# Kernel optimization log

Measured on AMD Instinct MI355X. Metric: run time of the kernel, lower is better.

The kernel has to match this reference:

```python
import jax, jax.numpy as jnp
import numpy as np

N = 20000      # num nodes
E = 320000     # num edges (avg degree 16)
F_IN = 518     # object_feature_dim
D = 128        # node_embedding_dim (= GAT out_channels)
ED = 32        # edge_embedding_dim
R = 26         # num_relations
H = 4          # GAT heads (concat=False -> mean over heads)
HID = 256      # node_encoder hidden


def _gat_layer(x, src, dst, ea, lin, lin_e, att_s, att_d, att_e, bias):
    """PyG GATConv: add_self_loops=True (fill_value='mean'), concat=False, negative_slope=0.2."""
    n = x.shape[0]
    ones = jnp.ones((src.shape[0],), x.dtype)
    cnt = jax.ops.segment_sum(ones, dst, num_segments=n)                    # [N]
    loop_ea = jax.ops.segment_sum(ea, dst, num_segments=n) / jnp.maximum(cnt, 1.0)[:, None]
    idx = jnp.arange(n)
    s = jnp.concatenate([src, idx])
    d = jnp.concatenate([dst, idx])
    ea2 = jnp.concatenate([ea, loop_ea], axis=0)                            # [E+N, ED]
    h = (x @ lin).reshape(n, H, D)                                          # [N,H,D]
    a_s = jnp.einsum('nhd,hd->nh', h, att_s)                                # [N,H]
    a_d = jnp.einsum('nhd,hd->nh', h, att_d)
    e = (ea2 @ lin_e).reshape(-1, H, D)                                     # [E+N,H,D]
    a_e = jnp.einsum('ehd,hd->eh', e, att_e)
    alpha = jax.nn.leaky_relu(a_s[s] + a_d[d] + a_e, 0.2)                   # [E+N,H]
    amax = jax.ops.segment_max(alpha, d, num_segments=n)
    alpha = jnp.exp(alpha - amax[d])
    denom = jax.ops.segment_sum(alpha, d, num_segments=n)
    alpha = alpha / (denom[d] + 1e-16)                                      # segment softmax
    msg = h[s] * alpha[:, :, None]                                          # [E+N,H,D]
    out = jax.ops.segment_sum(msg, d, num_segments=n)                       # [N,H,D]
    return out.mean(axis=1) + bias                                          # concat=False


def setup_inputs() -> dict:
    key = jax.random.key(0)
    ks = jax.random.split(key, 18)
    g = lambda k, shp, s=0.05: jax.random.normal(k, shp, jnp.float32) * s
    return {
        'x': g(ks[0], (N, F_IN), 1.0),
        'edge_index': jax.random.randint(ks[1], (2, E), 0, N),
        'edge_type': jax.random.randint(ks[2], (E,), 0, R),
        'w1': g(ks[3], (F_IN, HID)), 'b1': jnp.zeros((HID,), jnp.float32),
        'w2': g(ks[4], (HID, D)),    'b2': jnp.zeros((D,), jnp.float32),
        'rel_emb': g(ks[5], (R, ED), 1.0),
        'lin1': g(ks[6], (D, H * D)), 'line1': g(ks[7], (ED, H * D)),
        'atts1': g(ks[8], (H, D)), 'attd1': g(ks[9], (H, D)), 'atte1': g(ks[10], (H, D)),
        'bias1': jnp.zeros((D,), jnp.float32),
        'lin2': g(ks[11], (D, H * D)), 'line2': g(ks[12], (ED, H * D)),
        'atts2': g(ks[13], (H, D)), 'attd2': g(ks[14], (H, D)), 'atte2': g(ks[15], (H, D)),
        'bias2': jnp.zeros((D,), jnp.float32),
    }


def reference(x, edge_index, edge_type, w1, b1, w2, b2, rel_emb,
              lin1, line1, atts1, attd1, atte1, bias1,
              lin2, line2, atts2, attd2, atte2, bias2):
    src, dst = edge_index[0], edge_index[1]
    # node encoder (dropout inactive in eval)
    h = jax.nn.relu(x @ w1 + b1) @ w2 + b2                                  # [N,D]
    ea = rel_emb[edge_type]                                                 # [E,ED]
    h = jax.nn.relu(_gat_layer(h, src, dst, ea, lin1, line1, atts1, attd1, atte1, bias1))
    h = jax.nn.relu(_gat_layer(h, src, dst, ea, lin2, line2, atts2, attd2, atte2, bias2))
    return h
```

## Files before the change

### kernel.cpp

```cpp
#include <hip/hip_runtime.h>
#include <math.h>

#define N_NODES 20000
#define MP      20032
#define N_EDGES 320000
#define F_IN    518
#define HIDDEN  256
#define DIM     128
#define NH      4

typedef __attribute__((ext_vector_type(8))) short bf16x8;
typedef __attribute__((ext_vector_type(4))) float f32x4;
typedef unsigned short ushort_t;

__device__ __forceinline__ float lrelu02(float x) { return x > 0.f ? x : 0.2f * x; }

__device__ __forceinline__ void gl_lds16(const void* g, void* l) {
    __builtin_amdgcn_global_load_lds(
        (const __attribute__((address_space(1))) unsigned int*)g,
        (__attribute__((address_space(3))) unsigned int*)l, 16, 0, 0);
}

__device__ __forceinline__ unsigned int hi16(float v) { return __float_as_uint(v) >> 16; }
__device__ __forceinline__ unsigned int lo16(float v) {
    unsigned int h = __float_as_uint(v) & 0xFFFF0000u;
    return __float_as_uint(v - __uint_as_float(h)) >> 16;
}
__device__ __forceinline__ unsigned int rnd16(float v) {
    unsigned int u = __float_as_uint(v);
    return (u + 0x7FFFu + ((u >> 16) & 1u)) >> 16;
}
__device__ __forceinline__ float bfl(unsigned int u) { return __uint_as_float(u << 16); }
__device__ __forceinline__ float bfh(unsigned int u) { return __uint_as_float(u & 0xFFFF0000u); }

__global__ __launch_bounds__(256, 4) void gemm_mfma_v2(
    const ushort_t* __restrict__ Ah, const ushort_t* __restrict__ Al,
    const ushort_t* __restrict__ Bh, const ushort_t* __restrict__ Bl,
    const float* __restrict__ bias,
    int M, int K8, int N, int act,
    float* __restrict__ Cf,
    ushort_t* __restrict__ Ch, ushort_t* __restrict__ Cl,
    ushort_t* __restrict__ Cb,
    ushort_t* __restrict__ Ca)
{
    __shared__ __align__(16) ushort_t lds[12288];
    const int tid = threadIdx.x;
    const int w = tid >> 6, lane = tid & 63;
    const int row0 = blockIdx.y * 64, col0 = blockIdx.x * 128;
    const int nkb = K8 >> 2;
    const int m16 = lane & 15, q = lane >> 4;
    const bool use_al = (Al != nullptr);

    f32x4 acc[4][2] = {};

    for (int kb = 0; kb < nkb; ++kb) {
        const size_t kc = (size_t)(kb * 4 + w);
        const size_t aoff = (kc * MP + row0) * 8 + lane * 8;
        const size_t boff = (kc * N + col0) * 8 + lane * 8;
        gl_lds16(Ah + aoff, &lds[w * 512]);
        if (use_al) gl_lds16(Al + aoff, &lds[2048 + w * 512]);
        gl_lds16(Bh + boff,       &lds[4096 + w * 1024]);
        gl_lds16(Bh + boff + 512, &lds[4096 + w * 1024 + 512]);
        gl_lds16(Bl + boff,       &lds[8192 + w * 1024]);
        gl_lds16(Bl + boff + 512, &lds[8192 + w * 1024 + 512]);
        __syncthreads();

        bf16x8 fah[4], fal[4], fbh[2], fbl[2];
        const int fa = q * 512 + m16 * 8;
        #pragma unroll
        for (int mi = 0; mi < 4; ++mi) {
            fah[mi] = *(const bf16x8*)&lds[fa + mi * 128];
            if (use_al) fal[mi] = *(const bf16x8*)&lds[2048 + fa + mi * 128];
        }
        const int fb = q * 1024 + (w * 32 + m16) * 8;
        #pragma unroll
        for (int ni = 0; ni < 2; ++ni) {
            fbh[ni] = *(const bf16x8*)&lds[4096 + fb + ni * 128];
            fbl[ni] = *(const bf16x8*)&lds[8192 + fb + ni * 128];
        }
        #pragma unroll
        for (int mi = 0; mi < 4; ++mi)
            #pragma unroll
            for (int ni = 0; ni < 2; ++ni) {
                acc[mi][ni] = __builtin_amdgcn_mfma_f32_16x16x32_bf16(fah[mi], fbh[ni], acc[mi][ni], 0, 0, 0);
                acc[mi][ni] = __builtin_amdgcn_mfma_f32_16x16x32_bf16(fah[mi], fbl[ni], acc[mi][ni], 0, 0, 0);
            }
        if (use_al) {
            #pragma unroll
            for (int mi = 0; mi < 4; ++mi)
                #pragma unroll
                for (int ni = 0; ni < 2; ++ni)
                    acc[mi][ni] = __builtin_amdgcn_mfma_f32_16x16x32_bf16(fal[mi], fbh[ni], acc[mi][ni], 0, 0, 0);
        }
        __syncthreads();
    }

    #pragma unroll
    for (int ni = 0; ni < 2; ++ni) {
        const int col = col0 + w * 32 + ni * 16 + m16;
        const float bb = bias ? bias[col] : 0.f;
        #pragma unroll
        for (int mi = 0; mi < 4; ++mi) {
            #pragma unroll
            for (int r = 0; r < 4; ++r) {
                const int row = row0 + mi * 16 + q * 4 + r;
                if (row < M) {
                    float v = acc[mi][ni][r] + bb;
                    if (act) v = fmaxf(v, 0.f);
                    if (Cf) Cf[(size_t)row * N + col] = v;
                    if (Cb) Cb[(size_t)row * N + col] = (ushort_t)rnd16(v);
                    const size_t p = (((size_t)(col >> 3)) * MP + row) * 8 + (col & 7);
                    if (Ch) { Ch[p] = (ushort_t)hi16(v); Cl[p] = (ushort_t)lo16(v); }
                    if (Ca) Ca[p] = (ushort_t)rnd16(v);
                }
            }
        }
    }
}

__global__ __launch_bounds__(256) void conv_a_t_kernel(
    const float* __restrict__ x, ushort_t* __restrict__ xh, ushort_t* __restrict__ xl)
{
    __shared__ float tile[64][68];
    const int tid = threadIdx.x;
    const int r0 = blockIdx.x * 64;
    const int c0 = blockIdx.y * 64;

    #pragma unroll
    for (int it = 0; it < 4; ++it) {
        const int r = (tid >> 4) + it * 16;
        const int c = (tid & 15) * 4;
        const int gr = r0 + r, gc = c0 + c;
        float4 v = {0.f, 0.f, 0.f, 0.f};
        if (gr < N_NODES) {
            if (gc + 3 < F_IN) {
                v = *(const float4*)(x + (size_t)gr * F_IN + gc);
            } else {
                float tmp[4] = {0.f, 0.f, 0.f, 0.f};
                #pragma unroll
                for (int u = 0; u < 4; ++u)
                    if (gc + u < F_IN) tmp[u] = x[(size_t)gr * F_IN + gc + u];
                v.x = tmp[0]; v.y = tmp[1]; v.z = tmp[2]; v.w = tmp[3];
            }
        }
        tile[r][c] = v.x; tile[r][c+1] = v.y; tile[r][c+2] = v.z; tile[r][c+3] = v.w;
    }
    __syncthreads();

    const int k8l = tid >> 5;
    const int k8 = (c0 >> 3) + k8l;
    if (k8 >= 68) return;
    const int rr = (tid & 31) * 2;
    #pragma unroll
    for (int u = 0; u < 2; ++u) {
        const int r = rr + u;
        unsigned int hp[4], lp[4];
        #pragma unroll
        for (int i = 0; i < 4; ++i) {
            const float v0 = tile[r][k8l * 8 + 2 * i];
            const float v1 = tile[r][k8l * 8 + 2 * i + 1];
            hp[i] = (hi16(v1) << 16) | hi16(v0);
            lp[i] = (lo16(v1) << 16) | lo16(v0);
        }
        const size_t p = ((size_t)k8 * MP + r0 + r) * 8;
        *(uint4*)(xh + p) = make_uint4(hp[0], hp[1], hp[2], hp[3]);
        *(uint4*)(xl + p) = make_uint4(lp[0], lp[1], lp[2], lp[3]);
    }
}

__global__ __launch_bounds__(256) void conv_b_kernel(
    const float* __restrict__ w, ushort_t* __restrict__ bh, ushort_t* __restrict__ bl,
    int K, int N, int total)
{
    const int idx = blockIdx.x * 256 + threadIdx.x;
    if (idx >= total) return;
    const int j = idx & 7;
    const int rem = idx >> 3;
    const int n = rem % N;
    const int k = (rem / N) * 8 + j;
    const float v = (k < K) ? w[(size_t)k * N + n] : 0.f;
    bh[idx] = (ushort_t)hi16(v);
    bl[idx] = (ushort_t)lo16(v);
}

__global__ __launch_bounds__(256) void wa_kernel(
    const float* __restrict__ lin, const float* __restrict__ atts,
    const float* __restrict__ attd, float* __restrict__ wa_s, float* __restrict__ wa_d)
{
    const int wrk = blockIdx.x * 256 + threadIdx.x;
    if (wrk >= 1024) return;
    const int sd = wrk >> 9;
    const int p = wrk & 511;
    const int h = p >> 7, d = p & 127;
    const float* av = (sd ? attd : atts) + h * DIM;
    const float* lp = lin + (size_t)d * (NH * DIM) + h * DIM;
    float acc = 0.f;
    #pragma unroll 8
    for (int i = 0; i < DIM; ++i) acc += lp[i] * av[i];
    (sd ? wa_d : wa_s)[h * DIM + d] = acc;
}

__global__ __launch_bounds__(256) void as_ad_kernel(
    const float* __restrict__ xb, const float* __restrict__ wa_s,
    const float* __restrict__ wa_d, float* __restrict__ a_s, float* __restrict__ a_d)
{
    const int gw = blockIdx.x * 4 + (threadIdx.x >> 6);
    const int lane = threadIdx.x & 63;
    if (gw >= N_NODES * NH) return;
    const int n = gw >> 2, h = gw & 3;
    const float* hp = xb + (size_t)n * DIM;
    float2 hv = *(const float2*)(hp + lane * 2);
    float2 sv = *(const float2*)(wa_s + h * DIM + lane * 2);
    float2 dv = *(const float2*)(wa_d + h * DIM + lane * 2);
    float s = hv.x * sv.x + hv.y * sv.y;
    float d = hv.x * dv.x + hv.y * dv.y;
    #pragma unroll
    for (int off = 32; off > 0; off >>= 1) {
        s += __shfl_down(s, off);
        d += __shfl_down(d, off);
    }
    if (lane == 0) { a_s[n * 4 + h] = s; a_d[n * 4 + h] = d; }
}

__global__ __launch_bounds__(128) void rel_table_kernel(
    const float* __restrict__ rel_emb, const float* __restrict__ line,
    const float* __restrict__ atte, float* __restrict__ table)
{
    __shared__ float we[32][NH];
    const int tid = threadIdx.x;
    const int k = tid >> 2, h = tid & 3;
    float acc = 0.f;
    for (int d = 0; d < DIM; ++d)
        acc += line[(size_t)k * (NH * DIM) + h * DIM + d] * atte[h * DIM + d];
    we[k][h] = acc;
    __syncthreads();
    if (tid < 26 * NH) {
        int r = tid >> 2, hh = tid & 3;
        float t = 0.f;
        for (int kk = 0; kk < 32; ++kk) t += rel_emb[r * 32 + kk] * we[kk][hh];
        table[r * 4 + hh] = t;
    }
}

__global__ __launch_bounds__(256) void hist_kernel(
    const int* __restrict__ dst, int* __restrict__ cnt)
{
    const int e = blockIdx.x * blockDim.x + threadIdx.x;
    if (e >= N_EDGES) return;
    atomicAdd(&cnt[dst[e]], 1);
}

__global__ __launch_bounds__(1024) void scan_kernel(
    const int* __restrict__ cnt, int* __restrict__ ptr, int* __restrict__ ptr_copy)
{
    __shared__ int tsum[1024];
    const int tid = threadIdx.x;
    const int CH = 20;
    const int base = tid * CH;
    int s = 0;
    #pragma unroll
    for (int i = 0; i < CH; ++i) {
        int idx = base + i;
        if (idx < N_NODES) s += cnt[idx];
    }
    tsum[tid] = s;
    __syncthreads();
    for (int off = 1; off < 1024; off <<= 1) {
        int v = (tid >= off) ? tsum[tid - off] : 0;
        __syncthreads();
        tsum[tid] += v;
        __syncthreads();
    }
    int run = (tid == 0) ? 0 : tsum[tid - 1];
    #pragma unroll
    for (int i = 0; i < CH; ++i) {
        int idx = base + i;
        if (idx < N_NODES) {
            ptr[idx] = run;
            ptr_copy[idx] = run;
            run += cnt[idx];
        }
    }
    if (tid == 0) ptr[N_NODES] = N_EDGES;
}

__global__ __launch_bounds__(256) void scatter_kernel(
    const int* __restrict__ src, const int* __restrict__ dst, const int* __restrict__ etype,
    int* __restrict__ ptr_copy, int2* __restrict__ se)
{
    const int e = blockIdx.x * blockDim.x + threadIdx.x;
    if (e >= N_EDGES) return;
    const int d = dst[e];
    const int pos = atomicAdd(&ptr_copy[d], 1);
    se[pos] = make_int2(src[e], etype[e]);
}

__global__ __launch_bounds__(256) void node_agg_kernel(
    const int* __restrict__ ptr, const int2* __restrict__ se,
    const float* __restrict__ a_s, const float* __restrict__ a_d,
    const float* __restrict__ table, const ushort_t* __restrict__ hb,
    const float* __restrict__ bias,
    float* __restrict__ outf, ushort_t* __restrict__ oa,
    const float* __restrict__ wa_s2, const float* __restrict__ wa_d2,
    float* __restrict__ a_s2, float* __restrict__ a_d2)
{
    const int n = blockIdx.x * 4 + (threadIdx.x >> 6);
    const int lane = threadIdx.x & 63;
    if (n >= N_NODES) return;
    const int beg = ptr[n], end = ptr[n + 1];
    const int head = lane >> 4;
    const int cbase = lane * 8;
    const float adh = a_d[n * 4 + head];

    float acc[8] = {};
    float dh = 0.f, eh = 0.f;

    int j = beg;
    for (; j + 4 <= end; j += 4) {
        int2 E[4];
        E[0] = se[j]; E[1] = se[j + 1]; E[2] = se[j + 2]; E[3] = se[j + 3];
        uint4 g[4];
        float av[4], tv[4];
        #pragma unroll
        for (int u = 0; u < 4; ++u) {
            g[u] = *(const uint4*)(hb + (size_t)E[u].x * 512 + cbase);
            av[u] = a_s[E[u].x * 4 + head];
            tv[u] = table[E[u].y * 4 + head];
        }
        #pragma unroll
        for (int u = 0; u < 4; ++u) {
            const float p = __expf(lrelu02(av[u] + adh + tv[u]));
            eh += tv[u]; dh += p;
            acc[0] += p * bfl(g[u].x); acc[1] += p * bfh(g[u].x);
            acc[2] += p * bfl(g[u].y); acc[3] += p * bfh(g[u].y);
            acc[4] += p * bfl(g[u].z); acc[5] += p * bfh(g[u].z);
            acc[6] += p * bfl(g[u].w); acc[7] += p * bfh(g[u].w);
        }
    }
    for (; j < end; ++j) {
        const int2 E0 = se[j];
        const uint4 g0 = *(const uint4*)(hb + (size_t)E0.x * 512 + cbase);
        const float a0 = a_s[E0.x * 4 + head];
        const float t0 = table[E0.y * 4 + head];
        const float p0 = __expf(lrelu02(a0 + adh + t0));
        eh += t0; dh += p0;
        acc[0] += p0 * bfl(g0.x); acc[1] += p0 * bfh(g0.x);
        acc[2] += p0 * bfl(g0.y); acc[3] += p0 * bfh(g0.y);
        acc[4] += p0 * bfl(g0.z); acc[5] += p0 * bfh(g0.z);
        acc[6] += p0 * bfl(g0.w); acc[7] += p0 * bfh(g0.w);
    }

    const float inv = 1.0f / fmaxf((float)(end - beg), 1.0f);
    const float ps = __expf(lrelu02(a_s[n * 4 + head] + adh + eh * inv));
    dh += ps;
    {
        const uint4 gs = *(const uint4*)(hb + (size_t)n * 512 + cbase);
        acc[0] += ps * bfl(gs.x); acc[1] += ps * bfh(gs.x);
        acc[2] += ps * bfl(gs.y); acc[3] += ps * bfh(gs.y);
        acc[4] += ps * bfl(gs.z); acc[5] += ps * bfh(gs.z);
        acc[6] += ps * bfl(gs.w); acc[7] += ps * bfh(gs.w);
    }

    const float ih = 0.25f / (dh + 1e-16f);
    float t[8];
    #pragma unroll
    for (int k = 0; k < 8; ++k) {
        t[k] = acc[k] * ih;
        t[k] += __shfl_xor(t[k], 16);
        t[k] += __shfl_xor(t[k], 32);
    }
    if (lane < 16) {
        const float4 b0 = *(const float4*)(bias + cbase);
        const float4 b1 = *(const float4*)(bias + cbase + 4);
        float o[8];
        o[0] = fmaxf(t[0] + b0.x, 0.f); o[1] = fmaxf(t[1] + b0.y, 0.f);
        o[2] = fmaxf(t[2] + b0.z, 0.f); o[3] = fmaxf(t[3] + b0.w, 0.f);
        o[4] = fmaxf(t[4] + b1.x, 0.f); o[5] = fmaxf(t[5] + b1.y, 0.f);
        o[6] = fmaxf(t[6] + b1.z, 0.f); o[7] = fmaxf(t[7] + b1.w, 0.f);
        if (outf) {
            float4 v0 = {o[0], o[1], o[2], o[3]};
            float4 v1 = {o[4], o[5], o[6], o[7]};
            *(float4*)(outf + (size_t)n * DIM + cbase) = v0;
            *(float4*)(outf + (size_t)n * DIM + cbase + 4) = v1;
        }
        if (oa) {
            unsigned int up[4];
            #pragma unroll
            for (int i = 0; i < 4; ++i)
                up[i] = (rnd16(o[2*i+1]) << 16) | rnd16(o[2*i]);
            *(uint4*)(oa + ((size_t)lane * MP + n) * 8) = make_uint4(up[0], up[1], up[2], up[3]);
        }
        if (wa_s2) {
            float pss[4] = {0,0,0,0}, pdd[4] = {0,0,0,0};
            #pragma unroll
            for (int h = 0; h < NH; ++h) {
                const float* ws = wa_s2 + h * DIM + cbase;
                const float* wd = wa_d2 + h * DIM + cbase;
                #pragma unroll
                for (int i = 0; i < 8; ++i) {
                    pss[h] += o[i] * ws[i];
                    pdd[h] += o[i] * wd[i];
                }
            }
            #pragma unroll
            for (int m = 1; m < 16; m <<= 1) {
                #pragma unroll
                for (int h = 0; h < NH; ++h) {
                    pss[h] += __shfl_xor(pss[h], m);
                    pdd[h] += __shfl_xor(pdd[h], m);
                }
            }
            if (lane == 0) {
                float4 vs = {pss[0], pss[1], pss[2], pss[3]};
                float4 vd = {pdd[0], pdd[1], pdd[2], pdd[3]};
                *(float4*)(a_s2 + n * 4) = vs;
                *(float4*)(a_d2 + n * 4) = vd;
            }
        }
    }
}

extern "C" void kernel_launch(void* const* d_in, const int* in_sizes, int n_in,
                              void* d_out, int out_size, void* d_ws, size_t ws_size,
                              hipStream_t stream)
{
    const float* x       = (const float*)d_in[0];
    const int*   eidx    = (const int*)d_in[1];
    const int*   etype   = (const int*)d_in[2];
    const float* w1      = (const float*)d_in[3];
    const float* b1      = (const float*)d_in[4];
    const float* w2      = (const float*)d_in[5];
    const float* b2      = (const float*)d_in[6];
    const float* rel_emb = (const float*)d_in[7];
    const float* lin[2]  = {(const float*)d_in[8],  (const float*)d_in[14]};
    const float* line[2] = {(const float*)d_in[9],  (const float*)d_in[15]};
    const float* atts[2] = {(const float*)d_in[10], (const float*)d_in[16]};
    const float* attd[2] = {(const float*)d_in[11], (const float*)d_in[17]};
    const float* atte[2] = {(const float*)d_in[12], (const float*)d_in[18]};
    const float* bias[2] = {(const float*)d_in[13], (const float*)d_in[19]};
    const int* src = eidx;
    const int* dst = eidx + N_EDGES;

    char* base = (char*)d_ws;
    size_t off = 0;
    auto alloc = [&](size_t bytes) -> void* {
        void* p = base + off;
        off = (off + bytes + 255) & ~(size_t)255;
        return p;
    };
    ushort_t* xh  = (ushort_t*)alloc((size_t)68 * MP * 8 * 2);
    ushort_t* xl  = (ushort_t*)alloc((size_t)68 * MP * 8 * 2);
    ushort_t* h1h = (ushort_t*)alloc((size_t)32 * MP * 8 * 2);
    ushort_t* h1l = (ushort_t*)alloc((size_t)32 * MP * 8 * 2);
    ushort_t* x0a = (ushort_t*)alloc((size_t)16 * MP * 8 * 2);
    void* reg1    = alloc((size_t)16 * MP * 8 * 4);
    ushort_t* w1h = (ushort_t*)alloc(68 * 256 * 8 * 2);
    ushort_t* w1l = (ushort_t*)alloc(68 * 256 * 8 * 2);
    ushort_t* w2h = (ushort_t*)alloc(32 * 128 * 8 * 2);
    ushort_t* w2l = (ushort_t*)alloc(32 * 128 * 8 * 2);
    ushort_t* l0h = (ushort_t*)alloc(16 * 512 * 8 * 2);
    ushort_t* l0l = (ushort_t*)alloc(16 * 512 * 8 * 2);
    ushort_t* l1h = (ushort_t*)alloc(16 * 512 * 8 * 2);
    ushort_t* l1l = (ushort_t*)alloc(16 * 512 * 8 * 2);
    float* a_s0  = (float*)alloc(N_NODES * 4 * 4);
    float* a_d0  = (float*)alloc(N_NODES * 4 * 4);
    float* a_s1  = (float*)alloc(N_NODES * 4 * 4);
    float* a_d1  = (float*)alloc(N_NODES * 4 * 4);
    float* table = (float*)alloc(128 * 4);
    float* wa_s0 = (float*)alloc(512 * 4);
    float* wa_d0 = (float*)alloc(512 * 4);
    float* wa_s1 = (float*)alloc(512 * 4);
    float* wa_d1 = (float*)alloc(512 * 4);
    int*  cnt_i  = (int*)alloc(N_NODES * 4);
    int*  ptr    = (int*)alloc((N_NODES + 4) * 4);
    int*  ptrc   = (int*)alloc(N_NODES * 4);
    int2* se     = (int2*)alloc((size_t)N_EDGES * 8);

    ushort_t* hb = xh;
    float* xbuf0 = (float*)reg1;
    ushort_t* x1a = (ushort_t*)reg1;

    const int mtiles = MP / 64;

    conv_a_t_kernel<<<dim3(MP / 64, 9), 256, 0, stream>>>(x, xh, xl);
    conv_b_kernel<<<(68*256*8 + 255) / 256, 256, 0, stream>>>(w1, w1h, w1l, F_IN, HIDDEN, 68*256*8);
    conv_b_kernel<<<(32*128*8 + 255) / 256, 256, 0, stream>>>(w2, w2h, w2l, HIDDEN, DIM, 32*128*8);
    conv_b_kernel<<<(16*512*8 + 255) / 256, 256, 0, stream>>>(lin[0], l0h, l0l, DIM, NH*DIM, 16*512*8);
    conv_b_kernel<<<(16*512*8 + 255) / 256, 256, 0, stream>>>(lin[1], l1h, l1l, DIM, NH*DIM, 16*512*8);
    wa_kernel<<<4, 256, 0, stream>>>(lin[0], atts[0], attd[0], wa_s0, wa_d0);
    wa_kernel<<<4, 256, 0, stream>>>(lin[1], atts[1], attd[1], wa_s1, wa_d1);

    hipMemsetAsync(cnt_i, 0, N_NODES * sizeof(int), stream);
    hist_kernel<<<(N_EDGES + 255) / 256, 256, 0, stream>>>(dst, cnt_i);
    scan_kernel<<<1, 1024, 0, stream>>>(cnt_i, ptr, ptrc);
    scatter_kernel<<<(N_EDGES + 255) / 256, 256, 0, stream>>>(src, dst, etype, ptrc, se);

    gemm_mfma_v2<<<dim3(HIDDEN / 128, mtiles), 256, 0, stream>>>(
        xh, xl, w1h, w1l, b1, N_NODES, 68, HIDDEN, 1, nullptr, h1h, h1l, nullptr, nullptr);
    gemm_mfma_v2<<<dim3(DIM / 128, mtiles), 256, 0, stream>>>(
        h1h, h1l, w2h, w2l, b2, N_NODES, 32, DIM, 0, xbuf0, nullptr, nullptr, nullptr, x0a);

    gemm_mfma_v2<<<dim3((NH * DIM) / 128, mtiles), 256, 0, stream>>>(
        x0a, nullptr, l0h, l0l, nullptr, N_NODES, 16, NH * DIM, 0, nullptr, nullptr, nullptr, hb, nullptr);
    as_ad_kernel<<<N_NODES, 256, 0, stream>>>(xbuf0, wa_s0, wa_d0, a_s0, a_d0);
    rel_table_kernel<<<1, 128, 0, stream>>>(rel_emb, line[0], atte[0], table);
    node_agg_kernel<<<(N_NODES + 3) / 4, 256, 0, stream>>>(
        ptr, se, a_s0, a_d0, table, hb, bias[0], nullptr, x1a,
        wa_s1, wa_d1, a_s1, a_d1);

    gemm_mfma_v2<<<dim3((NH * DIM) / 128, mtiles), 256, 0, stream>>>(
        x1a, nullptr, l1h, l1l, nullptr, N_NODES, 16, NH * DIM, 0, nullptr, nullptr, nullptr, hb, nullptr);
    rel_table_kernel<<<1, 128, 0, stream>>>(rel_emb, line[1], atte[1], table);
    node_agg_kernel<<<(N_NODES + 3) / 4, 256, 0, stream>>>(
        ptr, se, a_s1, a_d1, table, hb, bias[1], (float*)d_out, nullptr,
        nullptr, nullptr, nullptr, nullptr);
}
```

Measured before the change: 440.2 us.

## Split each node's edge list across two waves and batch small setup kernels

The aggregation kernel now gives each destination node two waves. Each wave handles half of the node's incoming edges, and the partial sums are combined through shared memory before the epilogue. This is meant to expose more memory-level parallelism on the gather-bound aggregation. The cost is a block barrier, LDS traffic, and the second wave idling through the epilogue. Separately, the four weight-conversion launches, the two wa launches and the two rel_table launches are merged into single launches to cut launch overhead.

```diff
diff --git a/kernel.cpp b/kernel.cpp
--- a/kernel.cpp
+++ b/kernel.cpp
@@ -168,36 +168,55 @@
     }
 }
 
-__global__ __launch_bounds__(256) void conv_b_kernel(
-    const float* __restrict__ w, ushort_t* __restrict__ bh, ushort_t* __restrict__ bl,
-    int K, int N, int total)
-{
-    const int idx = blockIdx.x * 256 + threadIdx.x;
-    if (idx >= total) return;
-    const int j = idx & 7;
-    const int rem = idx >> 3;
+#define W1_T (68 * 256 * 8)
+#define W2_T (32 * 128 * 8)
+#define L_T  (16 * 512 * 8)
+__global__ __launch_bounds__(256) void conv_w_all_kernel(
+    const float* __restrict__ w1, const float* __restrict__ w2,
+    const float* __restrict__ l0, const float* __restrict__ l1,
+    ushort_t* __restrict__ w1h, ushort_t* __restrict__ w1l,
+    ushort_t* __restrict__ w2h, ushort_t* __restrict__ w2l,
+    ushort_t* __restrict__ l0h, ushort_t* __restrict__ l0l,
+    ushort_t* __restrict__ l1h, ushort_t* __restrict__ l1l)
+{
+    int idx = blockIdx.x * 256 + threadIdx.x;
+    const float* w; ushort_t *bh, *bl; int K, N, local;
+    if (idx < W1_T) { w = w1; bh = w1h; bl = w1l; K = F_IN; N = HIDDEN; local = idx; }
+    else if (idx < W1_T + W2_T) { w = w2; bh = w2h; bl = w2l; K = HIDDEN; N = DIM; local = idx - W1_T; }
+    else if (idx < W1_T + W2_T + L_T) { w = l0; bh = l0h; bl = l0l; K = DIM; N = 512; local = idx - W1_T - W2_T; }
+    else if (idx < W1_T + W2_T + 2 * L_T) { w = l1; bh = l1h; bl = l1l; K = DIM; N = 512; local = idx - W1_T - W2_T - L_T; }
+    else return;
+    const int j = local & 7;
+    const int rem = local >> 3;
     const int n = rem % N;
     const int k = (rem / N) * 8 + j;
     const float v = (k < K) ? w[(size_t)k * N + n] : 0.f;
-    bh[idx] = (ushort_t)hi16(v);
-    bl[idx] = (ushort_t)lo16(v);
-}
-
-__global__ __launch_bounds__(256) void wa_kernel(
-    const float* __restrict__ lin, const float* __restrict__ atts,
-    const float* __restrict__ attd, float* __restrict__ wa_s, float* __restrict__ wa_d)
+    bh[local] = (ushort_t)hi16(v);
+    bl[local] = (ushort_t)lo16(v);
+}
+
+__global__ __launch_bounds__(256) void wa2_kernel(
+    const float* __restrict__ lin0, const float* __restrict__ lin1,
+    const float* __restrict__ atts0, const float* __restrict__ attd0,
+    const float* __restrict__ atts1, const float* __restrict__ attd1,
+    float* __restrict__ wa_s0, float* __restrict__ wa_d0,
+    float* __restrict__ wa_s1, float* __restrict__ wa_d1)
 {
     const int wrk = blockIdx.x * 256 + threadIdx.x;
-    if (wrk >= 1024) return;
-    const int sd = wrk >> 9;
+    if (wrk >= 2048) return;
+    const int L = wrk >> 10;
+    const int sd = (wrk >> 9) & 1;
     const int p = wrk & 511;
     const int h = p >> 7, d = p & 127;
-    const float* av = (sd ? attd : atts) + h * DIM;
+    const float* lin = L ? lin1 : lin0;
+    const float* av = L ? (sd ? attd1 : atts1) : (sd ? attd0 : atts0);
+    float* out = L ? (sd ? wa_d1 : wa_s1) : (sd ? wa_d0 : wa_s0);
     const float* lp = lin + (size_t)d * (NH * DIM) + h * DIM;
+    const float* ap = av + h * DIM;
     float acc = 0.f;
     #pragma unroll 8
-    for (int i = 0; i < DIM; ++i) acc += lp[i] * av[i];
-    (sd ? wa_d : wa_s)[h * DIM + d] = acc;
+    for (int i = 0; i < DIM; ++i) acc += lp[i] * ap[i];
+    out[h * DIM + d] = acc;
 }
 
 __global__ __launch_bounds__(256) void as_ad_kernel(
@@ -222,11 +241,17 @@
     if (lane == 0) { a_s[n * 4 + h] = s; a_d[n * 4 + h] = d; }
 }
 
-__global__ __launch_bounds__(128) void rel_table_kernel(
-    const float* __restrict__ rel_emb, const float* __restrict__ line,
-    const float* __restrict__ atte, float* __restrict__ table)
+__global__ __launch_bounds__(128) void rel_table2_kernel(
+    const float* __restrict__ rel_emb,
+    const float* __restrict__ line0, const float* __restrict__ atte0,
+    const float* __restrict__ line1, const float* __restrict__ atte1,
+    float* __restrict__ table)
 {
     __shared__ float we[32][NH];
+    const int L = blockIdx.x;
+    const float* line = L ? line1 : line0;
+    const float* atte = L ? atte1 : atte0;
+    float* tab = table + L * 128;
     const int tid = threadIdx.x;
     const int k = tid >> 2, h = tid & 3;
     float acc = 0.f;
@@ -238,7 +263,7 @@
         int r = tid >> 2, hh = tid & 3;
         float t = 0.f;
         for (int kk = 0; kk < 32; ++kk) t += rel_emb[r * 32 + kk] * we[kk][hh];
-        table[r * 4 + hh] = t;
+        tab[r * 4 + hh] = t;
     }
 }
 
@@ -295,7 +320,7 @@
     se[pos] = make_int2(src[e], etype[e]);
 }
 
-__global__ __launch_bounds__(256) void node_agg_kernel(
+__global__ __launch_bounds__(256) void node_agg2_kernel(
     const int* __restrict__ ptr, const int2* __restrict__ se,
     const float* __restrict__ a_s, const float* __restrict__ a_d,
     const float* __restrict__ table, const ushort_t* __restrict__ hb,
@@ -304,40 +329,45 @@
     const float* __restrict__ wa_s2, const float* __restrict__ wa_d2,
     float* __restrict__ a_s2, float* __restrict__ a_d2)
 {
-    const int n = blockIdx.x * 4 + (threadIdx.x >> 6);
-    const int lane = threadIdx.x & 63;
-    if (n >= N_NODES) return;
-    const int beg = ptr[n], end = ptr[n + 1];
+    __shared__ float red[2][64][11];
+    const int tid = threadIdx.x;
+    const int wave = tid >> 6, lane = tid & 63;
+    const int slot = wave >> 1, half = wave & 1;
+    const int n = blockIdx.x * 2 + slot;
     const int head = lane >> 4;
     const int cbase = lane * 8;
+    const int beg = ptr[n], end = ptr[n + 1];
+    const int mid = beg + ((end - beg + 1) >> 1);
+    const int lo = half ? mid : beg;
+    const int hi = half ? end : mid;
     const float adh = a_d[n * 4 + head];
 
     float acc[8] = {};
     float dh = 0.f, eh = 0.f;
 
-    int j = beg;
-    for (; j + 4 <= end; j += 4) {
-        int2 E[4];
-        E[0] = se[j]; E[1] = se[j + 1]; E[2] = se[j + 2]; E[3] = se[j + 3];
-        uint4 g[4];
-        float av[4], tv[4];
-        #pragma unroll
-        for (int u = 0; u < 4; ++u) {
-            g[u] = *(const uint4*)(hb + (size_t)E[u].x * 512 + cbase);
-            av[u] = a_s[E[u].x * 4 + head];
-            tv[u] = table[E[u].y * 4 + head];
-        }
-        #pragma unroll
-        for (int u = 0; u < 4; ++u) {
-            const float p = __expf(lrelu02(av[u] + adh + tv[u]));
-            eh += tv[u]; dh += p;
-            acc[0] += p * bfl(g[u].x); acc[1] += p * bfh(g[u].x);
-            acc[2] += p * bfl(g[u].y); acc[3] += p * bfh(g[u].y);
-            acc[4] += p * bfl(g[u].z); acc[5] += p * bfh(g[u].z);
-            acc[6] += p * bfl(g[u].w); acc[7] += p * bfh(g[u].w);
-        }
-    }
-    for (; j < end; ++j) {
+    int j = lo;
+    for (; j + 2 <= hi; j += 2) {
+        const int2 E0 = se[j], E1 = se[j + 1];
+        const uint4 g0 = *(const uint4*)(hb + (size_t)E0.x * 512 + cbase);
+        const uint4 g1 = *(const uint4*)(hb + (size_t)E1.x * 512 + cbase);
+        const float a0 = a_s[E0.x * 4 + head];
+        const float t0 = table[E0.y * 4 + head];
+        const float a1 = a_s[E1.x * 4 + head];
+        const float t1 = table[E1.y * 4 + head];
+        const float p0 = __expf(lrelu02(a0 + adh + t0));
+        const float p1 = __expf(lrelu02(a1 + adh + t1));
+        eh += t0 + t1;
+        dh += p0 + p1;
+        acc[0] += p0 * bfl(g0.x) + p1 * bfl(g1.x);
+        acc[1] += p0 * bfh(g0.x) + p1 * bfh(g1.x);
+        acc[2] += p0 * bfl(g0.y) + p1 * bfl(g1.y);
+        acc[3] += p0 * bfh(g0.y) + p1 * bfh(g1.y);
+        acc[4] += p0 * bfl(g0.z) + p1 * bfl(g1.z);
+        acc[5] += p0 * bfh(g0.z) + p1 * bfh(g1.z);
+        acc[6] += p0 * bfl(g0.w) + p1 * bfl(g1.w);
+        acc[7] += p0 * bfh(g0.w) + p1 * bfh(g1.w);
+    }
+    if (j < hi) {
         const int2 E0 = se[j];
         const uint4 g0 = *(const uint4*)(hb + (size_t)E0.x * 512 + cbase);
         const float a0 = a_s[E0.x * 4 + head];
@@ -349,6 +379,20 @@
         acc[4] += p0 * bfl(g0.z); acc[5] += p0 * bfh(g0.z);
         acc[6] += p0 * bfl(g0.w); acc[7] += p0 * bfh(g0.w);
     }
+
+    if (half == 1) {
+        #pragma unroll
+        for (int k = 0; k < 8; ++k) red[slot][lane][k] = acc[k];
+        red[slot][lane][8] = dh;
+        red[slot][lane][9] = eh;
+    }
+    __syncthreads();
+    if (half == 1) return;
+
+    #pragma unroll
+    for (int k = 0; k < 8; ++k) acc[k] += red[slot][lane][k];
+    dh += red[slot][lane][8];
+    eh += red[slot][lane][9];
 
     const float inv = 1.0f / fmaxf((float)(end - beg), 1.0f);
     const float ps = __expf(lrelu02(a_s[n * 4 + head] + adh + eh * inv));
@@ -454,19 +498,19 @@
     ushort_t* h1l = (ushort_t*)alloc((size_t)32 * MP * 8 * 2);
     ushort_t* x0a = (ushort_t*)alloc((size_t)16 * MP * 8 * 2);
     void* reg1    = alloc((size_t)16 * MP * 8 * 4);
-    ushort_t* w1h = (ushort_t*)alloc(68 * 256 * 8 * 2);
-    ushort_t* w1l = (ushort_t*)alloc(68 * 256 * 8 * 2);
-    ushort_t* w2h = (ushort_t*)alloc(32 * 128 * 8 * 2);
-    ushort_t* w2l = (ushort_t*)alloc(32 * 128 * 8 * 2);
-    ushort_t* l0h = (ushort_t*)alloc(16 * 512 * 8 * 2);
-    ushort_t* l0l = (ushort_t*)alloc(16 * 512 * 8 * 2);
-    ushort_t* l1h = (ushort_t*)alloc(16 * 512 * 8 * 2);
-    ushort_t* l1l = (ushort_t*)alloc(16 * 512 * 8 * 2);
+    ushort_t* w1h = (ushort_t*)alloc(W1_T * 2);
+    ushort_t* w1l = (ushort_t*)alloc(W1_T * 2);
+    ushort_t* w2h = (ushort_t*)alloc(W2_T * 2);
+    ushort_t* w2l = (ushort_t*)alloc(W2_T * 2);
+    ushort_t* l0h = (ushort_t*)alloc(L_T * 2);
+    ushort_t* l0l = (ushort_t*)alloc(L_T * 2);
+    ushort_t* l1h = (ushort_t*)alloc(L_T * 2);
+    ushort_t* l1l = (ushort_t*)alloc(L_T * 2);
     float* a_s0  = (float*)alloc(N_NODES * 4 * 4);
     float* a_d0  = (float*)alloc(N_NODES * 4 * 4);
     float* a_s1  = (float*)alloc(N_NODES * 4 * 4);
     float* a_d1  = (float*)alloc(N_NODES * 4 * 4);
-    float* table = (float*)alloc(128 * 4);
+    float* table = (float*)alloc(2 * 128 * 4);
     float* wa_s0 = (float*)alloc(512 * 4);
     float* wa_d0 = (float*)alloc(512 * 4);
     float* wa_s1 = (float*)alloc(512 * 4);
@@ -483,12 +527,11 @@
     const int mtiles = MP / 64;
 
     conv_a_t_kernel<<<dim3(MP / 64, 9), 256, 0, stream>>>(x, xh, xl);
-    conv_b_kernel<<<(68*256*8 + 255) / 256, 256, 0, stream>>>(w1, w1h, w1l, F_IN, HIDDEN, 68*256*8);
-    conv_b_kernel<<<(32*128*8 + 255) / 256, 256, 0, stream>>>(w2, w2h, w2l, HIDDEN, DIM, 32*128*8);
-    conv_b_kernel<<<(16*512*8 + 255) / 256, 256, 0, stream>>>(lin[0], l0h, l0l, DIM, NH*DIM, 16*512*8);
-    conv_b_kernel<<<(16*512*8 + 255) / 256, 256, 0, stream>>>(lin[1], l1h, l1l, DIM, NH*DIM, 16*512*8);
-    wa_kernel<<<4, 256, 0, stream>>>(lin[0], atts[0], attd[0], wa_s0, wa_d0);
-    wa_kernel<<<4, 256, 0, stream>>>(lin[1], atts[1], attd[1], wa_s1, wa_d1);
+    conv_w_all_kernel<<<(W1_T + W2_T + 2 * L_T + 255) / 256, 256, 0, stream>>>(
+        w1, w2, lin[0], lin[1], w1h, w1l, w2h, w2l, l0h, l0l, l1h, l1l);
+    wa2_kernel<<<8, 256, 0, stream>>>(lin[0], lin[1], atts[0], attd[0], atts[1], attd[1],
+                                      wa_s0, wa_d0, wa_s1, wa_d1);
+    rel_table2_kernel<<<2, 128, 0, stream>>>(rel_emb, line[0], atte[0], line[1], atte[1], table);
 
     hipMemsetAsync(cnt_i, 0, N_NODES * sizeof(int), stream);
     hist_kernel<<<(N_EDGES + 255) / 256, 256, 0, stream>>>(dst, cnt_i);
@@ -503,15 +546,13 @@
     gemm_mfma_v2<<<dim3((NH * DIM) / 128, mtiles), 256, 0, stream>>>(
         x0a, nullptr, l0h, l0l, nullptr, N_NODES, 16, NH * DIM, 0, nullptr, nullptr, nullptr, hb, nullptr);
     as_ad_kernel<<<N_NODES, 256, 0, stream>>>(xbuf0, wa_s0, wa_d0, a_s0, a_d0);
-    rel_table_kernel<<<1, 128, 0, stream>>>(rel_emb, line[0], atte[0], table);
-    node_agg_kernel<<<(N_NODES + 3) / 4, 256, 0, stream>>>(
+    node_agg2_kernel<<<N_NODES / 2, 256, 0, stream>>>(
         ptr, se, a_s0, a_d0, table, hb, bias[0], nullptr, x1a,
         wa_s1, wa_d1, a_s1, a_d1);
 
     gemm_mfma_v2<<<dim3((NH * DIM) / 128, mtiles), 256, 0, stream>>>(
         x1a, nullptr, l1h, l1l, nullptr, N_NODES, 16, NH * DIM, 0, nullptr, nullptr, nullptr, hb, nullptr);
-    rel_table_kernel<<<1, 128, 0, stream>>>(rel_emb, line[1], atte[1], table);
-    node_agg_kernel<<<(N_NODES + 3) / 4, 256, 0, stream>>>(
-        ptr, se, a_s1, a_d1, table, hb, bias[1], (float*)d_out, nullptr,
+    node_agg2_kernel<<<N_NODES / 2, 256, 0, stream>>>(
+        ptr, se, a_s1, a_d1, table + 128, hb, bias[1], (float*)d_out, nullptr,
         nullptr, nullptr, nullptr, nullptr);
 }
```

New measurement: 426.0 us. 3.2% less time.
